# Kernel optimization log

Hardware: AMD Instinct MI355X
Metric: run time of the kernel (lower is better)

## Reference

```python
import jax, jax.numpy as jnp
import numpy as np

B, T, N_EMBED, HEAD_SIZE = 8, 2048, 1024, 64
NEG_INF = float('-inf')


def setup_inputs() -> dict:
    key = jax.random.key(0)
    ks = jax.random.split(key, 6)
    k = jax.random.normal(ks[0], (B, T, N_EMBED), dtype=jnp.float32)
    q = jax.random.normal(ks[1], (B, T, N_EMBED), dtype=jnp.float32)
    v = jax.random.normal(ks[2], (B, T, N_EMBED), dtype=jnp.float32)
    mask = jnp.ones((B, T), dtype=jnp.int32)  # 1 = attendable key position
    scale = 1.0 / np.sqrt(N_EMBED)  # keep logits well-scaled
    Wk = jax.random.normal(ks[3], (HEAD_SIZE, N_EMBED), dtype=jnp.float32) * scale
    Wq = jax.random.normal(ks[4], (HEAD_SIZE, N_EMBED), dtype=jnp.float32) * scale
    Wv = jax.random.normal(ks[5], (HEAD_SIZE, N_EMBED), dtype=jnp.float32) * scale
    return {"k": k, "q": q, "v": v, "mask": mask, "Wk": Wk, "Wq": Wq, "Wv": Wv}


def reference(k, q, v, mask, Wk, Wq, Wv):
    # Linear projections (bias=False): x @ W.T, W is [head_size, n_embed]
    kh = jnp.einsum('btd,hd->bth', k, Wk)  # [B,T,H]
    qh = jnp.einsum('btd,hd->bth', q, Wq)  # [B,T,H]
    vh = jnp.einsum('btd,hd->bth', v, Wv)  # [B,T,H]

    # Scaled scores: q @ k^T * head_size**-0.5 -> [B,T,T]
    wei = jnp.einsum('bqh,bkh->bqk', qh, kh) * (HEAD_SIZE ** -0.5)

    # Causal (look-ahead) mask
    Tq = k.shape[1]
    causal = jnp.tril(jnp.ones((Tq, Tq), dtype=bool))
    wei = jnp.where(causal[None, :, :], wei, NEG_INF)

    # Custom key mask: mask [B,T] broadcast over query dim (mask.unsqueeze(1))
    wei = jnp.where(mask[:, None, :] == 0, NEG_INF, wei)

    wei = jax.nn.softmax(wei, axis=-1)
    # dropout p=0.0 -> identity
    out = jnp.einsum('bqk,bkh->bqh', wei, vh)  # [B,T,H]
    return out
```

## Files before the change

### kernel.cpp

```cpp
#include <hip/hip_runtime.h>
#include <hip/hip_bf16.h>

#define NB 8
#define NT 2048
#define NE 1024
#define NH 64

typedef __bf16 bf16_t;
typedef __bf16 bf16x8 __attribute__((ext_vector_type(8)));
typedef float f32x4 __attribute__((ext_vector_type(4)));

#define MFMA16(a, b, c) __builtin_amdgcn_mfma_f32_16x16x32_bf16(a, b, c, 0, 0, 0)

static __device__ __forceinline__ f32x4 fzero4() {
    f32x4 z = {0.f, 0.f, 0.f, 0.f};
    return z;
}

static __device__ __forceinline__ void gload_lds16(const void* gsrc, void* ldst) {
    __builtin_amdgcn_global_load_lds(
        (const __attribute__((address_space(1))) char*)gsrc,
        (__attribute__((address_space(3))) char*)ldst, 16, 0, 0);
}

__global__ __launch_bounds__(256) void convw_kernel(
    const float* __restrict__ Wq, const float* __restrict__ Wk,
    const float* __restrict__ Wv, bf16_t* __restrict__ Wb)
{
    int src = blockIdx.y;
    const float* W = (src == 0) ? Wq : ((src == 1) ? Wk : Wv);
    int idx = (blockIdx.x * 256 + threadIdx.x) * 8;
    f32x4 a = *(const f32x4*)(W + idx);
    f32x4 b = *(const f32x4*)(W + idx + 4);
    bf16x8 o;
#pragma unroll
    for (int j = 0; j < 4; ++j) { o[j] = (bf16_t)a[j]; o[4 + j] = (bf16_t)b[j]; }
    *(bf16x8*)(Wb + (size_t)src * (NH * NE) + idx) = o;
}

__global__ __launch_bounds__(256) void proj_kernel(
    const float* __restrict__ q_in, const float* __restrict__ k_in,
    const float* __restrict__ v_in, const bf16_t* __restrict__ Wb,
    bf16_t* __restrict__ qh, bf16_t* __restrict__ kh, bf16_t* __restrict__ vhT)
{
    const int which = blockIdx.y;
    const int w    = threadIdx.x >> 6;
    const int lane = threadIdx.x & 63;
    const int l15  = lane & 15;
    const int lhi  = lane >> 4;
    const int t0   = blockIdx.x * 64;

    const float*  x = (which == 0) ? q_in : ((which == 1) ? k_in : v_in);
    const bf16_t* W = Wb + (size_t)which * (NH * NE);

    __shared__ __align__(16) char xlds[2][4][2048];
    __shared__ __align__(16) char wlds[2][4096];

    const float* xsrc[2];
#pragma unroll
    for (int i = 0; i < 2; ++i) {
        int rw   = i * 8 + (lane >> 3);
        int phys = lane & 7;
        xsrc[i] = x + (size_t)(t0 + w * 16 + rw) * NE + ((phys ^ (rw & 7)) << 2);
    }
    const bf16_t* wsrc = W + (size_t)lane * NE + w * 8;

    int xo[2];
#pragma unroll
    for (int j = 0; j < 2; ++j)
        xo[j] = l15 * 128 + ((((lhi * 2 + j) ^ (l15 & 7))) << 4);
    int wo[4];
#pragma unroll
    for (int cg = 0; cg < 4; ++cg)
        wo[cg] = lhi * 1024 + (cg * 16 + l15) * 16;

    f32x4 acc[4] = {fzero4(), fzero4(), fzero4(), fzero4()};

    gload_lds16(xsrc[0], &xlds[0][w][0]);
    gload_lds16(xsrc[1], &xlds[0][w][1024]);
    gload_lds16(wsrc, &wlds[0][w * 1024]);
    __syncthreads();

#pragma unroll 4
    for (int step = 0; step < 32; ++step) {
        const int cur = step & 1;
        if (step < 31) {
            const int k0 = (step + 1) * 32;
            gload_lds16(xsrc[0] + k0, &xlds[cur ^ 1][w][0]);
            gload_lds16(xsrc[1] + k0, &xlds[cur ^ 1][w][1024]);
            gload_lds16(wsrc + k0, &wlds[cur ^ 1][w * 1024]);
        }
        const char* xb = xlds[cur][w];
        const char* wb = wlds[cur];

        f32x4 a0 = *(const f32x4*)(xb + xo[0]);
        f32x4 a1 = *(const f32x4*)(xb + xo[1]);
        bf16x8 xf;
#pragma unroll
        for (int j = 0; j < 4; ++j) { xf[j] = (bf16_t)a0[j]; xf[4 + j] = (bf16_t)a1[j]; }

        if (which < 2) {
            acc[0] = MFMA16(xf, *(const bf16x8*)(wb + wo[0]), acc[0]);
            acc[1] = MFMA16(xf, *(const bf16x8*)(wb + wo[1]), acc[1]);
            acc[2] = MFMA16(xf, *(const bf16x8*)(wb + wo[2]), acc[2]);
            acc[3] = MFMA16(xf, *(const bf16x8*)(wb + wo[3]), acc[3]);
        } else {
            acc[0] = MFMA16(*(const bf16x8*)(wb + wo[0]), xf, acc[0]);
            acc[1] = MFMA16(*(const bf16x8*)(wb + wo[1]), xf, acc[1]);
            acc[2] = MFMA16(*(const bf16x8*)(wb + wo[2]), xf, acc[2]);
            acc[3] = MFMA16(*(const bf16x8*)(wb + wo[3]), xf, acc[3]);
        }
        __syncthreads();
    }

    if (which < 2) {
        bf16_t* outp = (which == 0) ? qh : kh;
#pragma unroll
        for (int cg = 0; cg < 4; ++cg)
#pragma unroll
            for (int r = 0; r < 4; ++r) {
                int t = t0 + w * 16 + lhi * 4 + r;
                outp[(size_t)t * NH + cg * 16 + l15] = (bf16_t)acc[cg][r];
            }
    } else {
        const int tg = t0 + w * 16 + l15;
        const int b  = tg >> 11;
        const int tt = tg & 2047;
#pragma unroll
        for (int hg = 0; hg < 4; ++hg)
#pragma unroll
            for (int r = 0; r < 4; ++r) {
                int h = hg * 16 + lhi * 4 + r;
                vhT[(((size_t)(b * NH + h)) << 11) + tt] = (bf16_t)acc[hg][r];
            }
    }
}

__global__ __launch_bounds__(256) void attn_kernel(
    const bf16_t* __restrict__ qh, const bf16_t* __restrict__ kh,
    const bf16_t* __restrict__ vhT, const int* __restrict__ mask,
    float* __restrict__ out)
{
    const int lin  = blockIdx.x;
    const int qt16 = lin >> 3;
    const int b    = lin & 7;
    const int w    = threadIdx.x >> 6;
    const int lane = threadIdx.x & 63;
    const int l15  = lane & 15;
    const int lhi  = lane >> 4;

    __shared__ __align__(16) char plds[4][2][2048];
    __shared__ float sm_o[4][16][65];
    __shared__ float sm_ml[4][2][16];

    const int q0  = qt16 * 16;
    const int nkt = (q0 + 15) / 64 + 1;
    const int len = (nkt + 3) >> 2;
    const int kt_beg = w * len;
    const int kt_end = min(kt_beg + len, nkt);

    const bf16_t* qbase = qh + (size_t)(b * NT + q0 + l15) * NH + lhi * 8;
    bf16x8 qf0 = *(const bf16x8*)(qbase);
    bf16x8 qf1 = *(const bf16x8*)(qbase + 32);

    f32x4 acc_o[4] = {fzero4(), fzero4(), fzero4(), fzero4()};
    float m[4]    = {-1e30f, -1e30f, -1e30f, -1e30f};
    float lsum[4] = {0.f, 0.f, 0.f, 0.f};

    const int qq0 = q0 + lhi * 4;

    for (int kt = kt_beg; kt < kt_end; ++kt) {
        const bf16_t* kbase = kh + (size_t)(b * NT + kt * 64 + l15) * NH + lhi * 8;
        f32x4 s[4] = {fzero4(), fzero4(), fzero4(), fzero4()};
#pragma unroll
        for (int cg = 0; cg < 4; ++cg) {
            bf16x8 kf0 = *(const bf16x8*)(kbase + (size_t)cg * 16 * NH);
            bf16x8 kf1 = *(const bf16x8*)(kbase + (size_t)cg * 16 * NH + 32);
            s[cg] = MFMA16(qf0, kf0, s[cg]);
            s[cg] = MFMA16(qf1, kf1, s[cg]);
        }

        int mk[4];
#pragma unroll
        for (int cg = 0; cg < 4; ++cg) mk[cg] = mask[b * NT + kt * 64 + cg * 16 + l15];
#pragma unroll
        for (int cg = 0; cg < 4; ++cg) {
            int kk = kt * 64 + cg * 16 + l15;
#pragma unroll
            for (int r = 0; r < 4; ++r) {
                float sv = s[cg][r] * 0.125f;
                bool ok = (kk <= qq0 + r) && (mk[cg] != 0);
                s[cg][r] = ok ? sv : -1e30f;
            }
        }

        float mx[4];
#pragma unroll
        for (int r = 0; r < 4; ++r) {
            mx[r] = fmaxf(fmaxf(s[0][r], s[1][r]), fmaxf(s[2][r], s[3][r]));
#pragma unroll
            for (int d = 1; d < 16; d <<= 1) mx[r] = fmaxf(mx[r], __shfl_xor(mx[r], d));
        }
        float resc[4];
#pragma unroll
        for (int r = 0; r < 4; ++r) {
            float mn = fmaxf(m[r], mx[r]);
            resc[r] = __expf(m[r] - mn);
            m[r] = mn;
        }
        float rs[4] = {0.f, 0.f, 0.f, 0.f};
#pragma unroll
        for (int cg = 0; cg < 4; ++cg)
#pragma unroll
            for (int r = 0; r < 4; ++r) {
                float sv = s[cg][r];
                float p = (sv > -5e29f) ? __expf(sv - m[r]) : 0.f;
                s[cg][r] = p;
                rs[r] += p;
            }
#pragma unroll
        for (int r = 0; r < 4; ++r) {
#pragma unroll
            for (int d = 1; d < 16; d <<= 1) rs[r] += __shfl_xor(rs[r], d);
            lsum[r] = lsum[r] * resc[r] + rs[r];
        }
#pragma unroll
        for (int cg = 0; cg < 4; ++cg)
#pragma unroll
            for (int r = 0; r < 4; ++r) acc_o[cg][r] *= resc[r];

        char* pb = &plds[w][kt & 1][0];
#pragma unroll
        for (int cg = 0; cg < 4; ++cg)
#pragma unroll
            for (int r = 0; r < 4; ++r) {
                int row = lhi * 4 + r;
                int col = cg * 16 + l15;
                int byte = (row * 128 + col * 2) ^ ((row & 7) << 4);
                *(bf16_t*)(pb + byte) = (bf16_t)s[cg][r];
            }

        const bf16_t* vbase = vhT + ((size_t)(b * NH + l15) << 11) + kt * 64 + lhi * 8;
#pragma unroll
        for (int kc = 0; kc < 2; ++kc) {
            int row = l15;
            int byte = (row * 128 + kc * 64 + lhi * 16) ^ ((row & 7) << 4);
            bf16x8 pf = *(bf16x8*)(pb + byte);
#pragma unroll
            for (int cg = 0; cg < 4; ++cg) {
                bf16x8 vf = *(const bf16x8*)(vbase + ((size_t)cg * 16 << 11) + kc * 32);
                acc_o[cg] = MFMA16(pf, vf, acc_o[cg]);
            }
        }
    }

#pragma unroll
    for (int cg = 0; cg < 4; ++cg)
#pragma unroll
        for (int r = 0; r < 4; ++r)
            sm_o[w][lhi * 4 + r][cg * 16 + l15] = acc_o[cg][r];
    if (l15 == 0) {
#pragma unroll
        for (int r = 0; r < 4; ++r) {
            sm_ml[w][0][lhi * 4 + r] = m[r];
            sm_ml[w][1][lhi * 4 + r] = lsum[r];
        }
    }
    __syncthreads();

#pragma unroll
    for (int r = 0; r < 4; ++r) {
        int row = lhi * 4 + r;
        float mg = -1e30f;
#pragma unroll
        for (int s = 0; s < 4; ++s) mg = fmaxf(mg, sm_ml[s][0][row]);
        float lg = 0.f, og = 0.f;
#pragma unroll
        for (int s = 0; s < 4; ++s) {
            float e = __expf(sm_ml[s][0][row] - mg);
            lg += e * sm_ml[s][1][row];
            og += e * sm_o[s][row][w * 16 + l15];
        }
        out[(size_t)(b * NT + q0 + row) * NH + w * 16 + l15] = og / lg;
    }
}

extern "C" void kernel_launch(void* const* d_in, const int* in_sizes, int n_in,
                              void* d_out, int out_size, void* d_ws, size_t ws_size,
                              hipStream_t stream)
{
    const float* k_in = (const float*)d_in[0];
    const float* q_in = (const float*)d_in[1];
    const float* v_in = (const float*)d_in[2];
    const int*   mask = (const int*)d_in[3];
    const float* Wk   = (const float*)d_in[4];
    const float* Wq   = (const float*)d_in[5];
    const float* Wv   = (const float*)d_in[6];
    float* out = (float*)d_out;

    char* ws = (char*)d_ws;
    bf16_t* Wb  = (bf16_t*)ws;
    bf16_t* qh  = (bf16_t*)(ws + 3 * NH * NE * 2);
    bf16_t* kh  = qh + (size_t)NB * NT * NH;
    bf16_t* vhT = kh + (size_t)NB * NT * NH;

    convw_kernel<<<dim3(32, 3), 256, 0, stream>>>(Wq, Wk, Wv, Wb);
    proj_kernel<<<dim3(NB * NT / 64, 3), 256, 0, stream>>>(q_in, k_in, v_in, Wb, qh, kh, vhT);
    attn_kernel<<<dim3(NB * NT / 16), 256, 0, stream>>>(qh, kh, vhT, mask, out);
}
```

Baseline: 85.17 us.

## Deepen projection load pipeline to four LDS stages with explicit vmcnt waits

The projection kernel's global-to-LDS staging goes from a two-buffer ring to a four-buffer ring, issuing loads two steps ahead. Each step now waits with a manual s_waitcnt vmcnt count plus a raw s_barrier instead of a full __syncthreads, and the loop is fully unrolled. The aim is to keep more memory traffic in flight and hide load latency on this memory-bound projection. It doubles LDS use, which may reduce occupancy. It also drops the trailing barrier, relying on the four-slot ring distance to avoid overwriting a buffer while it is still being read.

Result: slower. 89.79 us (+5.4%).

```diff
diff --git a/kernel.cpp b/kernel.cpp
--- a/kernel.cpp
+++ b/kernel.cpp
@@ -53,8 +53,8 @@
     const float*  x = (which == 0) ? q_in : ((which == 1) ? k_in : v_in);
     const bf16_t* W = Wb + (size_t)which * (NH * NE);
 
-    __shared__ __align__(16) char xlds[2][4][2048];
-    __shared__ __align__(16) char wlds[2][4096];
+    __shared__ __align__(16) char xlds[4][4][2048];
+    __shared__ __align__(16) char wlds[4][4096];
 
     const float* xsrc[2];
 #pragma unroll
@@ -76,22 +76,27 @@
 
     f32x4 acc[4] = {fzero4(), fzero4(), fzero4(), fzero4()};
 
-    gload_lds16(xsrc[0], &xlds[0][w][0]);
-    gload_lds16(xsrc[1], &xlds[0][w][1024]);
-    gload_lds16(wsrc, &wlds[0][w * 1024]);
-    __syncthreads();
-
-#pragma unroll 4
-    for (int step = 0; step < 32; ++step) {
-        const int cur = step & 1;
-        if (step < 31) {
-            const int k0 = (step + 1) * 32;
-            gload_lds16(xsrc[0] + k0, &xlds[cur ^ 1][w][0]);
-            gload_lds16(xsrc[1] + k0, &xlds[cur ^ 1][w][1024]);
-            gload_lds16(wsrc + k0, &wlds[cur ^ 1][w * 1024]);
-        }
-        const char* xb = xlds[cur][w];
-        const char* wb = wlds[cur];
+#define ISSUE_STEP(s)                                                        \
+    do {                                                                     \
+        const int k0_ = (s) * 32;                                            \
+        gload_lds16(xsrc[0] + k0_, &xlds[(s) & 3][w][0]);                    \
+        gload_lds16(xsrc[1] + k0_, &xlds[(s) & 3][w][1024]);                 \
+        gload_lds16(wsrc + k0_, &wlds[(s) & 3][w * 1024]);                   \
+    } while (0)
+
+    ISSUE_STEP(0);
+    ISSUE_STEP(1);
+
+#pragma unroll
+    for (int s = 0; s < 32; ++s) {
+        if (s < 30) ISSUE_STEP(s + 2);
+        if (s < 30)       asm volatile("s_waitcnt vmcnt(6)" ::: "memory");
+        else if (s == 30) asm volatile("s_waitcnt vmcnt(3)" ::: "memory");
+        else              asm volatile("s_waitcnt vmcnt(0)" ::: "memory");
+        __builtin_amdgcn_s_barrier();
+
+        const char* xb = xlds[s & 3][w];
+        const char* wb = wlds[s & 3];
 
         f32x4 a0 = *(const f32x4*)(xb + xo[0]);
         f32x4 a1 = *(const f32x4*)(xb + xo[1]);
@@ -110,8 +115,8 @@
             acc[2] = MFMA16(*(const bf16x8*)(wb + wo[2]), xf, acc[2]);
             acc[3] = MFMA16(*(const bf16x8*)(wb + wo[3]), xf, acc[3]);
         }
-        __syncthreads();
-    }
+    }
+#undef ISSUE_STEP
 
     if (which < 2) {
         bf16_t* outp = (which == 0) ? qh : kh;
```
